# Kernel optimization log

Measured on AMD Instinct MI355X. Metric: run time of the kernel, lower is better.

Reference implementation:

```python
import jax, jax.numpy as jnp
import numpy as np

NODE_NUM = 2048
DIM_IN = 2
DIM_OUT = 64
CHEB_K = 2
EMBED_DIM = 16
BATCH = 16


def _sagc(x, E, w_pool, b_pool):
    """AGCRN-style adaptive graph conv. x: [B,N,C]; E: [N,e];
    w_pool: [e,K,C,O]; b_pool: [e,O]. Returns (out [B,N,O], A [N,N])."""
    n = E.shape[0]
    A = E @ E.T                                   # [N,N] raw (signed) similarity
    supports = jax.nn.softmax(jax.nn.relu(A), axis=1)
    s_list = [jnp.eye(n, dtype=x.dtype), supports]
    for _ in range(2, CHEB_K):
        s_list.append(2.0 * supports @ s_list[-1] - s_list[-2])
    S = jnp.stack(s_list[:CHEB_K])                # [K,N,N]
    W = jnp.einsum('ne,ekio->nkio', E, w_pool)    # per-node weights [N,K,C,O]
    b = E @ b_pool                                # [N,O]
    x_g = jnp.einsum('knm,bmi->bnki', S, x)       # [B,N,K,C]
    out = jnp.einsum('bnki,nkio->bno', x_g, W) + b
    return out, A


def _degrees(adj_mask, H, weight):
    """adj_mask: [N,N] {0,1}; H: [B,N,D]; weight: [N,N] -> softmaxed [B,N,N]."""
    HHT = jnp.einsum('bnd,bmd->bnm', H, H)        # [B,N,N]
    AHHT = adj_mask * HHT                          # broadcast [N,N]*[B,N,N]
    AHHTW = jnp.einsum('bnm,mk->bnk', AHHT, weight)
    return jax.nn.softmax(AHHTW, axis=-1)


def setup_inputs() -> dict:
    key = jax.random.key(0)
    ks = jax.random.split(key, 9)
    din = DIM_IN + DIM_OUT
    return {
        'x': jax.random.normal(ks[0], (BATCH, NODE_NUM, DIM_IN), jnp.float32),
        'state': jax.random.normal(ks[1], (BATCH, NODE_NUM, DIM_OUT), jnp.float32),
        'node_embeddings': jax.random.normal(ks[2], (NODE_NUM, EMBED_DIM), jnp.float32) * 0.5,
        'weight_connect': jax.random.normal(ks[3], (NODE_NUM, NODE_NUM), jnp.float32) * 0.02,
        'weight_disconnect': jax.random.normal(ks[4], (NODE_NUM, NODE_NUM), jnp.float32) * 0.02,
        'gate_w': jax.random.normal(ks[5], (EMBED_DIM, CHEB_K, din, 2 * DIM_OUT), jnp.float32) * 0.05,
        'gate_b': jax.random.normal(ks[6], (EMBED_DIM, 2 * DIM_OUT), jnp.float32) * 0.05,
        'upd_w': jax.random.normal(ks[7], (EMBED_DIM, CHEB_K, din, DIM_OUT), jnp.float32) * 0.05,
        'upd_b': jax.random.normal(ks[8], (EMBED_DIM, DIM_OUT), jnp.float32) * 0.05,
    }


def reference(x, state, node_embeddings, weight_connect, weight_disconnect,
              gate_w, gate_b, upd_w, upd_b):
    inp = jnp.concatenate([x, state], axis=-1)            # [B,N,Cin+D]
    x_gconv, A = _sagc(inp, node_embeddings, gate_w, gate_b)
    z_r = jax.nn.sigmoid(x_gconv)
    z, r = jnp.split(z_r, 2, axis=-1)
    candidate = jnp.concatenate([x, z * state], axis=-1)
    hc = jnp.tanh(_sagc(candidate, node_embeddings, upd_w, upd_b)[0])
    h = r * state + (1.0 - r) * hc                        # [B,N,D]
    A_connect = jnp.where(A > 0, 1.0, 0.0).astype(h.dtype)
    A_disconnect = jnp.where(A < 0, 1.0, 0.0).astype(h.dtype)
    deg_c = _degrees(A_connect, h, weight_connect)        # [B,N,N]
    deg_d = _degrees(A_disconnect, h, weight_disconnect)
    numerator = (0.8 * h
                 - 0.1 * jnp.einsum('bnm,bmd->bnd', deg_c, h)
                 + 0.1 * jnp.einsum('bnm,bmd->bnd', deg_d, h))
    return numerator
```

## Files before the change

### kernel.cpp

```cpp
#include <hip/hip_runtime.h>
#include <hip/hip_bf16.h>

typedef unsigned short u16;
typedef unsigned int   u32;
typedef unsigned char  u8;

typedef __attribute__((ext_vector_type(8))) short bf16x8;
typedef __attribute__((ext_vector_type(4))) float f32x4;
typedef __attribute__((ext_vector_type(16))) float f32x16;

static __device__ __forceinline__ float bf2f(u16 u){ return __uint_as_float(((u32)u)<<16); }
static __device__ __forceinline__ u16 f2bf(float f){
  u32 u = __float_as_uint(f);
  u32 r = (u + 0x7fff + ((u>>16)&1)) >> 16;
  return (u16)r;
}

static __device__ __forceinline__ u8 f2fp8(float v){
  v = fminf(440.f, fmaxf(-440.f, v));
  return (u8)(__builtin_amdgcn_cvt_pk_fp8_f32(v, 0.f, 0, false) & 0xff);
}
static __device__ __forceinline__ u32 pk4_fp8(float a, float b, float c, float d){
  int w = __builtin_amdgcn_cvt_pk_fp8_f32(a, b, 0, false);
  w = __builtin_amdgcn_cvt_pk_fp8_f32(c, d, w, true);
  return (u32)w;
}

static __device__ __forceinline__ f32x4 mfma_bf16(bf16x8 a, bf16x8 b, f32x4 c){
  return __builtin_amdgcn_mfma_f32_16x16x32_bf16(a, b, c, 0, 0, 0);
}
static __device__ __forceinline__ f32x16 mfma_bf16_32(bf16x8 a, bf16x8 b, f32x16 c){
  return __builtin_amdgcn_mfma_f32_32x32x16_bf16(a, b, c, 0, 0, 0);
}
static __device__ __forceinline__ f32x16 mfma_fp8_32(long a, long b, f32x16 c){
  return __builtin_amdgcn_mfma_f32_32x32x16_fp8_fp8(a, b, c, 0, 0, 0);
}
static __device__ __forceinline__ long lo64(uint4 v){ return (long)(((unsigned long long)v.y<<32) | v.x); }
static __device__ __forceinline__ long hi64(uint4 v){ return (long)(((unsigned long long)v.w<<32) | v.z); }
static __device__ __forceinline__ long mklong(u32 lo, u32 hi){ return (long)(((unsigned long long)hi<<32) | lo); }

__global__ void k_w8(const float* __restrict__ Wc, const float* __restrict__ Wd,
                     u8* __restrict__ Wc8, u8* __restrict__ Wd8){
  __shared__ float tile[64][65];
  const float* src = blockIdx.z ? Wd : Wc;
  u8* dst = blockIdx.z ? Wd8 : Wc8;
  const int m0 = blockIdx.x*64, k0 = blockIdx.y*64;
  const int t = threadIdx.x, r = t & 63, cc = t >> 6;
  #pragma unroll
  for (int j=0;j<4;j++){
    float4 v = *(const float4*)&src[(size_t)(m0+r)*2048 + k0 + cc*16 + j*4];
    tile[r][cc*16+j*4+0]=v.x; tile[r][cc*16+j*4+1]=v.y;
    tile[r][cc*16+j*4+2]=v.z; tile[r][cc*16+j*4+3]=v.w;
  }
  __syncthreads();
  const int lane = t & 63, sub = t >> 6;
  const int kth = sub & 1, mcp = sub >> 1;
  const int kl = kth*32 + (lane & 31);
  const int ml = mcp*32 + (lane >> 5)*8;
  u32 b0 = pk4_fp8(16.f*tile[ml+ 0][kl], 16.f*tile[ml+ 1][kl], 16.f*tile[ml+ 2][kl], 16.f*tile[ml+ 3][kl]);
  u32 b1 = pk4_fp8(16.f*tile[ml+ 4][kl], 16.f*tile[ml+ 5][kl], 16.f*tile[ml+ 6][kl], 16.f*tile[ml+ 7][kl]);
  u32 b2 = pk4_fp8(16.f*tile[ml+16][kl], 16.f*tile[ml+17][kl], 16.f*tile[ml+18][kl], 16.f*tile[ml+19][kl]);
  u32 b3 = pk4_fp8(16.f*tile[ml+20][kl], 16.f*tile[ml+21][kl], 16.f*tile[ml+22][kl], 16.f*tile[ml+23][kl]);
  const int pt = m0 >> 6, kt = (k0 >> 5) + kth;
  u8* dbase = dst + (size_t)((pt*64 + kt)*2 + mcp)*1024 + lane*16;
  *(uint4*)dbase = make_uint4(b0, b1, b2, b3);
}

__global__ void k_hcvt(const float* __restrict__ h, u16* __restrict__ hb16,
                       u8* __restrict__ ht8p, u16* __restrict__ hfm){
  __shared__ float tile[64][65];
  const int k0 = blockIdx.x*64, b = blockIdx.y;
  const int t = threadIdx.x, r = t & 63, cc = t >> 6;
  const float* src = h + ((size_t)b*2048 + k0)*64;
  u32 hw[8];
  #pragma unroll
  for (int j=0;j<4;j++){
    float4 v = *(const float4*)&src[(size_t)r*64 + cc*16 + j*4];
    tile[r][cc*16+j*4+0]=v.x; tile[r][cc*16+j*4+1]=v.y;
    tile[r][cc*16+j*4+2]=v.z; tile[r][cc*16+j*4+3]=v.w;
    hw[2*j]   = (u32)f2bf(v.x) | ((u32)f2bf(v.y)<<16);
    hw[2*j+1] = (u32)f2bf(v.z) | ((u32)f2bf(v.w)<<16);
  }
  u16* hp = hb16 + (((size_t)b*2048 + k0 + r)*64 + cc*16);
  *(uint4*)hp     = make_uint4(hw[0],hw[1],hw[2],hw[3]);
  *(uint4*)(hp+8) = make_uint4(hw[4],hw[5],hw[6],hw[7]);
  __syncthreads();
  {
    const int lane = t & 63, sub = cc;
    const int k16 = (k0 >> 4) + sub;
    const int lr = sub*16 + ((lane >> 5) << 3);
    const int d0 = lane & 31;
    #pragma unroll
    for (int dt=0; dt<2; ++dt){
      const int d = dt*32 + d0;
      u32 w0 = pk4_fp8(tile[lr+0][d], tile[lr+1][d], tile[lr+2][d], tile[lr+3][d]);
      u32 w1 = pk4_fp8(tile[lr+4][d], tile[lr+5][d], tile[lr+6][d], tile[lr+7][d]);
      *(uint2*)(ht8p + (size_t)b*131072 + (size_t)(k16*2 + dt)*512 + lane*8) = make_uint2(w0, w1);
    }
  }
  {
    const int col = k0 + r, ks = cc >> 1, q0 = (cc & 1)*2;
    const int ctg = col >> 4, lcv = col & 15;
    u16* fbase = hfm + (size_t)b*131072 + (size_t)ks*65536 + ((size_t)ctg*64)*8;
    #pragma unroll
    for (int qq=0; qq<2; ++qq){
      int q = q0 + qq;
      u32 p0 = (u32)f2bf(tile[r][ks*32+q*8+0]) | ((u32)f2bf(tile[r][ks*32+q*8+1])<<16);
      u32 p1 = (u32)f2bf(tile[r][ks*32+q*8+2]) | ((u32)f2bf(tile[r][ks*32+q*8+3])<<16);
      u32 p2 = (u32)f2bf(tile[r][ks*32+q*8+4]) | ((u32)f2bf(tile[r][ks*32+q*8+5])<<16);
      u32 p3 = (u32)f2bf(tile[r][ks*32+q*8+6]) | ((u32)f2bf(tile[r][ks*32+q*8+7])<<16);
      *(uint4*)(fbase + (size_t)(q*16 + lcv)*8) = make_uint4(p0,p1,p2,p3);
    }
  }
}

__global__ void k_P(const float* __restrict__ E, u16* __restrict__ P, u8* __restrict__ msk){
  __shared__ float Ew[16];
  __shared__ float arow[2048];
  __shared__ float red[4];
  const int t = threadIdx.x, n = blockIdx.x;
  if (t < 16) Ew[t] = E[n*16 + t];
  __syncthreads();
  float lmax = 0.f;
  for (int i=0;i<8;i++){
    int m = t + 256*i;
    const float* ep = E + m*16;
    float dot = 0.f;
    #pragma unroll
    for (int d=0; d<16; ++d) dot += Ew[d]*ep[d];
    msk[n*2048 + m] = dot > 0.f ? (u8)1 : (dot < 0.f ? (u8)2 : (u8)0);
    float ar = fmaxf(dot, 0.f);
    arow[m] = ar;
    lmax = fmaxf(lmax, ar);
  }
  for (int o=1;o<64;o<<=1) lmax = fmaxf(lmax, __shfl_xor(lmax, o));
  if ((t&63)==0) red[t>>6] = lmax;
  __syncthreads();
  float gmax = fmaxf(fmaxf(red[0],red[1]), fmaxf(red[2],red[3]));
  __syncthreads();
  float lsum = 0.f;
  for (int i=0;i<8;i++){
    int m = t + 256*i;
    float e = expf(arow[m] - gmax);
    arow[m] = e;
    lsum += e;
  }
  for (int o=1;o<64;o<<=1) lsum += __shfl_xor(lsum, o);
  if ((t&63)==0) red[t>>6] = lsum;
  __syncthreads();
  float inv = 1.f/(red[0]+red[1]+red[2]+red[3]);
  for (int i=0;i<8;i++){
    int m = t + 256*i;
    P[n*2048 + m] = f2bf(arow[m]*inv);
  }
}

__global__ void k_mbits(const u8* __restrict__ msk, u32* __restrict__ mp2, u32* __restrict__ mn2){
  const int m = blockIdx.x, nb = blockIdx.y*256;
  const int t = threadIdx.x, w = t>>6, lane = t&63;
  u8 v = msk[(size_t)(nb + t)*2048 + m];
  unsigned long long bp = __ballot(v == (u8)1);
  unsigned long long bn = __ballot(v == (u8)2);
  if (lane == 0){
    int wi = (nb + w*64) >> 5;
    mp2[(size_t)wi*2048 + m]     = (u32)bp;
    mp2[(size_t)(wi+1)*2048 + m] = (u32)(bp>>32);
    mn2[(size_t)wi*2048 + m]     = (u32)bn;
    mn2[(size_t)(wi+1)*2048 + m] = (u32)(bn>>32);
  }
}

__global__ void k_c1x(const u16* __restrict__ P, const float* __restrict__ x, float* __restrict__ c1x){
  const int t = threadIdx.x;
  const int r = t>>1, c = t&1;
  const int n = blockIdx.x*64 + r, b = blockIdx.y;
  const u16* pr = P + (size_t)n*2048;
  const float* xb = x + (size_t)b*2048*2 + c;
  float acc = 0.f;
  for (int m=0;m<2048;m+=4){
    acc += bf2f(pr[m+0])*xb[(m+0)*2];
    acc += bf2f(pr[m+1])*xb[(m+1)*2];
    acc += bf2f(pr[m+2])*xb[(m+2)*2];
    acc += bf2f(pr[m+3])*xb[(m+3)*2];
  }
  c1x[((size_t)b*2048 + n)*2 + c] = acc;
}

__global__ void k_conv(const u16* __restrict__ P, const float* __restrict__ Z, float* __restrict__ Y){
  __shared__ u16 Pt[64][68];
  __shared__ u16 Zhi[64][68];
  __shared__ u16 Zlo[64][68];
  const int t = threadIdx.x;
  const int w = t >> 6, lane = t & 63, l32 = lane & 31, h32 = lane >> 5;
  const int nh = w & 1, dh = w >> 1;
  const int n0 = blockIdx.x*64, b = blockIdx.y;
  const int mloc = t & 63, grp = t >> 6;
  f32x16 acch = (f32x16)(0.f), accl = (f32x16)(0.f);
  for (int mc = 0; mc < 32; ++mc){
    const int m0 = mc*64;
    {
      const u16* pp = P + (size_t)(n0 + mloc)*2048 + m0 + grp*16;
      uint4 v0 = *(const uint4*)pp;
      uint4 v1 = *(const uint4*)(pp + 8);
      *(uint4*)&Pt[mloc][grp*16]     = v0;
      *(uint4*)&Pt[mloc][grp*16 + 8] = v1;
      const float* zp = Z + ((size_t)b*2048 + m0 + mloc)*64 + grp*16;
      #pragma unroll
      for (int jj = 0; jj < 4; ++jj){
        float4 zv = *(const float4*)(zp + jj*4);
        const int dd = grp*16 + jj*4;
        u16 h0 = f2bf(zv.x); Zhi[dd+0][mloc] = h0; Zlo[dd+0][mloc] = f2bf(zv.x - bf2f(h0));
        u16 h1 = f2bf(zv.y); Zhi[dd+1][mloc] = h1; Zlo[dd+1][mloc] = f2bf(zv.y - bf2f(h1));
        u16 h2 = f2bf(zv.z); Zhi[dd+2][mloc] = h2; Zlo[dd+2][mloc] = f2bf(zv.z - bf2f(h2));
        u16 h3 = f2bf(zv.w); Zhi[dd+3][mloc] = h3; Zlo[dd+3][mloc] = f2bf(zv.w - bf2f(h3));
      }
    }
    __syncthreads();
    #pragma unroll
    for (int kt = 0; kt < 4; ++kt){
      bf16x8 a  = *(const bf16x8*)&Pt[nh*32 + l32][kt*16 + h32*8];
      bf16x8 bh = *(const bf16x8*)&Zhi[dh*32 + l32][kt*16 + h32*8];
      bf16x8 bl = *(const bf16x8*)&Zlo[dh*32 + l32][kt*16 + h32*8];
      acch = mfma_bf16_32(a, bh, acch);
      accl = mfma_bf16_32(a, bl, accl);
    }
    __syncthreads();
  }
  #pragma unroll
  for (int g = 0; g < 16; ++g){
    const int row = (g&3) + 8*(g>>2) + 4*h32;
    Y[((size_t)b*2048 + n0 + nh*32 + row)*64 + dh*32 + l32] = acch[g] + accl[g];
  }
}

__global__ void k_gate(const float* __restrict__ E, const float* __restrict__ gw, const float* __restrict__ gb,
                       const float* __restrict__ x, const float* __restrict__ state,
                       const float* __restrict__ c1x, const float* __restrict__ c1s,
                       float* __restrict__ zs, float* __restrict__ rws){
  __shared__ float Ew[16];
  __shared__ float bnv[128];
  __shared__ float Wn[2][66][64];
  __shared__ float xg4[4][2][66];
  const int t = threadIdx.x, n = blockIdx.x;
  if (t < 16) Ew[t] = E[n*16 + t];
  __syncthreads();
  if (t < 128){
    float a = 0.f;
    #pragma unroll
    for (int e=0;e<16;e++) a += Ew[e]*gb[e*128 + t];
    bnv[t] = a;
  }
  for (int half=0; half<2; ++half){
    for (int idx=t; idx<8448; idx+=256){
      int o = idx & 63, rest = idx>>6, i = rest % 66, k = rest / 66;
      float a = 0.f;
      #pragma unroll
      for (int e=0;e<16;e++) a += Ew[e]*gw[((e*2+k)*66 + i)*128 + half*64 + o];
      Wn[k][i][o] = a;
    }
    __syncthreads();
    for (int bb=0; bb<4; ++bb){
      for (int idx=t; idx<528; idx+=256){
        int bi = idx/132, rem = idx%132, k = rem/66, i = rem%66;
        int b = bb*4 + bi;
        float v;
        if (k==0) v = (i<2) ? x[((size_t)b*2048+n)*2 + i] : state[((size_t)b*2048+n)*64 + (i-2)];
        else      v = (i<2) ? c1x[((size_t)b*2048+n)*2 + i] : c1s[((size_t)b*2048+n)*64 + (i-2)];
        xg4[bi][k][i] = v;
      }
      __syncthreads();
      {
        int bi = t>>6, o = t&63, b = bb*4 + bi;
        float a = 0.f;
        #pragma unroll
        for (int k=0;k<2;k++)
          for (int i=0;i<66;i++) a += xg4[bi][k][i]*Wn[k][i][o];
        a += bnv[half*64 + o];
        float s = 1.f/(1.f + expf(-a));
        if (half==0) zs[((size_t)b*2048+n)*64 + o] = s*state[((size_t)b*2048+n)*64 + o];
        else         rws[((size_t)b*2048+n)*64 + o] = s;
      }
      __syncthreads();
    }
  }
}

__global__ void k_upd(const float* __restrict__ E, const float* __restrict__ uw, const float* __restrict__ ub,
                      const float* __restrict__ x, const float* __restrict__ state,
                      const float* __restrict__ zs, const float* __restrict__ c1x, const float* __restrict__ c2s,
                      const float* __restrict__ rws, float* __restrict__ h){
  __shared__ float Ew[16];
  __shared__ float bnu[64];
  __shared__ float Wn[2][66][64];
  __shared__ float xg4[4][2][66];
  const int t = threadIdx.x, n = blockIdx.x;
  if (t < 16) Ew[t] = E[n*16 + t];
  __syncthreads();
  if (t < 64){
    float a = 0.f;
    #pragma unroll
    for (int e=0;e<16;e++) a += Ew[e]*ub[e*64 + t];
    bnu[t] = a;
  }
  for (int idx=t; idx<8448; idx+=256){
    int o = idx & 63, rest = idx>>6, i = rest % 66, k = rest / 66;
    float a = 0.f;
    #pragma unroll
    for (int e=0;e<16;e++) a += Ew[e]*uw[((e*2+k)*66 + i)*64 + o];
    Wn[k][i][o] = a;
  }
  __syncthreads();
  for (int bb=0; bb<4; ++bb){
    for (int idx=t; idx<528; idx+=256){
      int bi = idx/132, rem = idx%132, k = rem/66, i = rem%66;
      int b = bb*4 + bi;
      float v;
      if (k==0) v = (i<2) ? x[((size_t)b*2048+n)*2 + i] : zs[((size_t)b*2048+n)*64 + (i-2)];
      else      v = (i<2) ? c1x[((size_t)b*2048+n)*2 + i] : c2s[((size_t)b*2048+n)*64 + (i-2)];
      xg4[bi][k][i] = v;
    }
    __syncthreads();
    {
      int bi = t>>6, o = t&63, b = bb*4 + bi;
      float a = 0.f;
      #pragma unroll
      for (int k=0;k<2;k++)
        for (int i=0;i<66;i++) a += xg4[bi][k][i]*Wn[k][i][o];
      float hc = tanhf(a + bnu[o]);
      float rv = rws[((size_t)b*2048+n)*64 + o];
      h[((size_t)b*2048+n)*64 + o] = rv*state[((size_t)b*2048+n)*64 + o] + (1.f - rv)*hc;
    }
    __syncthreads();
  }
}

static __device__ __forceinline__ void sm_step(f32x16& LK0, f32x16& LK1,
    f32x16& OA, f32x16& OB, float& mrun, float& srun,
    const u8* __restrict__ htb, int ktA, int ktB, int lane, int h32){
  const float LN256 = 5.545177444479562f;
  float cmax = LK0[0];
  #pragma unroll
  for (int g=1; g<16; ++g) cmax = fmaxf(cmax, LK0[g]);
  #pragma unroll
  for (int g=0; g<16; ++g) cmax = fmaxf(cmax, LK1[g]);
  cmax = fmaxf(cmax, __shfl_xor(cmax, 32));
  float mnew = fmaxf(mrun, 0.5f*cmax);
  float sc = __expf(mrun - mnew);
  srun *= sc;
  #pragma unroll
  for (int g=0; g<16; ++g){
    const int rowl = (g&3) + 8*(g>>2) + 4*h32;
    float fr = __shfl(sc, rowl);
    OA[g] *= fr; OB[g] *= fr;
  }
  float cs = 0.f;
  #pragma unroll
  for (int kti=0; kti<2; ++kti){
    const int kt = kti ? ktB : ktA;
    float p[16];
    #pragma unroll
    for (int g=0; g<16; ++g){
      float Lg = kti ? LK1[g] : LK0[g];
      p[g] = __expf(0.5f*Lg - mnew + LN256);
      cs += p[g];
    }
    u32 qA = pk4_fp8(p[0],p[1],p[2],p[3]);
    u32 qB = pk4_fp8(p[4],p[5],p[6],p[7]);
    u32 qC = pk4_fp8(p[8],p[9],p[10],p[11]);
    u32 qD = pk4_fp8(p[12],p[13],p[14],p[15]);
    u32 xA = __shfl_xor(qA,32), xB = __shfl_xor(qB,32);
    u32 xC = __shfl_xor(qC,32), xD = __shfl_xor(qD,32);
    long pf0 = h32 ? mklong(xB,qB) : mklong(qA,xA);
    long pf1 = h32 ? mklong(xD,qD) : mklong(qC,xC);
    long h00 = *(const long*)(htb + (size_t)((kt*2+0)*2 + 0)*512 + lane*8);
    long h01 = *(const long*)(htb + (size_t)((kt*2+0)*2 + 1)*512 + lane*8);
    long h10 = *(const long*)(htb + (size_t)((kt*2+1)*2 + 0)*512 + lane*8);
    long h11 = *(const long*)(htb + (size_t)((kt*2+1)*2 + 1)*512 + lane*8);
    OA = mfma_fp8_32(pf0, h00, OA);
    OB = mfma_fp8_32(pf0, h01, OB);
    OA = mfma_fp8_32(pf1, h10, OA);
    OB = mfma_fp8_32(pf1, h11, OB);
  }
  cs += __shfl_xor(cs, 32);
  srun += cs;
  mrun = mnew;
}

#define SROW8 2056

__global__ void __launch_bounds__(512,2) k_deg(
    const u32* __restrict__ mbits, const u16* __restrict__ hb16,
    const u8* __restrict__ W8,
    const u8* __restrict__ ht8p, const u16* __restrict__ hfm,
    const float* __restrict__ hf32, const float* __restrict__ oc_in,
    float* __restrict__ outp, int fin){
  extern __shared__ u8 S[];
  __shared__ float maxw[64][8];
  __shared__ float sumw[64][8];
  __shared__ float sgl_lds[64];
  const int t = threadIdx.x;
  const int w = t >> 6, lane = t & 63, lc = lane & 15, q = lane >> 4;
  const int l32 = lane & 31, h32 = lane >> 5;
  const int id = blockIdx.x;
  const int b = id >> 5, n0 = (id & 31) * 64;
  const int p0 = (id >> 3) & 31;
  const u32* mrow0 = mbits + (size_t)(n0 >> 5)*2048;
  const u32* mrow1 = mrow0 + 2048;
  const u16* hbb = hb16 + (size_t)b*2048*64;
  const u16* hfb = hfm + (size_t)b*131072;
  const u8* htb = ht8p + (size_t)b*131072;

  {
    const int c0 = p0 & 15;
    bf16x8 A[4][2];
    #pragma unroll
    for (int rt=0; rt<4; ++rt)
      #pragma unroll
      for (int ks=0; ks<2; ++ks)
        A[rt][ks] = *(const bf16x8*)&hbb[(size_t)(n0 + rt*16 + lc)*64 + ks*32 + q*8];
    int ctg0 = w*16 + c0;
    bf16x8 B0c = *(const bf16x8*)(hfb + (size_t)ctg0*512 + lane*8);
    bf16x8 B1c = *(const bf16x8*)(hfb + 65536 + (size_t)ctg0*512 + lane*8);
    u32 m0c = mrow0[ctg0*16 + lc], m1c = mrow1[ctg0*16 + lc];
    #pragma unroll 1
    for (int ct=0; ct<16; ++ct){
      const int ctg  = w*16 + ((ct + c0) & 15);
      const int ctgn = w*16 + ((ct + 1 + c0) & 15);
      bf16x8 B0n = *(const bf16x8*)(hfb + (size_t)ctgn*512 + lane*8);
      bf16x8 B1n = *(const bf16x8*)(hfb + 65536 + (size_t)ctgn*512 + lane*8);
      u32 m0n = mrow0[ctgn*16 + lc], m1n = mrow1[ctgn*16 + lc];
      const int mcol = ctg*16 + lc;
      f32x4 a[4];
      #pragma unroll
      for (int rt=0; rt<4; ++rt){
        a[rt] = (f32x4){0.f,0.f,0.f,0.f};
        a[rt] = mfma_bf16(A[rt][0], B0c, a[rt]);
        a[rt] = mfma_bf16(A[rt][1], B1c, a[rt]);
      }
      #pragma unroll
      for (int rt=0; rt<4; ++rt){
        const u32 mw = (rt < 2) ? m0c : m1c;
        #pragma unroll
        for (int i=0;i<4;i++){
          const int row = rt*16 + q*4 + i;
          float v = ((mw >> (row & 31)) & 1u) ? a[rt][i]*0.125f : 0.f;
          S[row*SROW8 + mcol] = f2fp8(v);
        }
      }
      B0c = B0n; B1c = B1n; m0c = m0n; m1c = m1n;
    }
  }
  __syncthreads();

  const u8* sb0 = S + (size_t)l32*SROW8 + h32*8;
  const u8* sb1 = S + (size_t)(32 + l32)*SROW8 + h32*8;
  const u8* wl = W8 + lane*16;
  f32x16 oA0 = (f32x16)(0.f), oA1 = (f32x16)(0.f);
  f32x16 oB0 = (f32x16)(0.f), oB1 = (f32x16)(0.f);
  float mrun0 = -1e30f, srun0 = 0.f, mrun1 = -1e30f, srun1 = 0.f;
  #pragma unroll 1
  for (int si = 0; si < 4; ++si){
    const int ktA = w*8 + si*2, ktB = ktA + 1;
    f32x16 L00 = (f32x16)(0.f), L01 = (f32x16)(0.f);
    f32x16 L10 = (f32x16)(0.f), L11 = (f32x16)(0.f);
    uint4 wv0, wv1, wv2, wv3;
    {
      const int pt0 = p0;
      wv0 = *(const uint4*)(wl + (size_t)((pt0*64 + ktA)*2 + 0)*1024);
      wv1 = *(const uint4*)(wl + (size_t)((pt0*64 + ktA)*2 + 1)*1024);
      wv2 = *(const uint4*)(wl + (size_t)((pt0*64 + ktB)*2 + 0)*1024);
      wv3 = *(const uint4*)(wl + (size_t)((pt0*64 + ktB)*2 + 1)*1024);
    }
    __builtin_amdgcn_s_setprio(1);
    #pragma unroll 1
    for (int pti = 0; pti < 32; ++pti){
      const int pt  = (pti + p0) & 31;
      const int ptn = (pti + 1 + p0) & 31;
      long b00 = *(const long*)(sb0 + pt*64 +  0);
      long b01 = *(const long*)(sb0 + pt*64 + 16);
      long b02 = *(const long*)(sb0 + pt*64 + 32);
      long b03 = *(const long*)(sb0 + pt*64 + 48);
      long b10 = *(const long*)(sb1 + pt*64 +  0);
      long b11 = *(const long*)(sb1 + pt*64 + 16);
      long b12 = *(const long*)(sb1 + pt*64 + 32);
      long b13 = *(const long*)(sb1 + pt*64 + 48);
      uint4 wn0 = *(const uint4*)(wl + (size_t)((ptn*64 + ktA)*2 + 0)*1024);
      uint4 wn1 = *(const uint4*)(wl + (size_t)((ptn*64 + ktA)*2 + 1)*1024);
      uint4 wn2 = *(const uint4*)(wl + (size_t)((ptn*64 + ktB)*2 + 0)*1024);
      uint4 wn3 = *(const uint4*)(wl + (size_t)((ptn*64 + ktB)*2 + 1)*1024);
      L00 = mfma_fp8_32(lo64(wv0), b00, L00);
      L01 = mfma_fp8_32(lo64(wv0), b10, L01);
      L10 = mfma_fp8_32(lo64(wv2), b00, L10);
      L11 = mfma_fp8_32(lo64(wv2), b10, L11);
      L00 = mfma_fp8_32(hi64(wv0), b01, L00);
      L01 = mfma_fp8_32(hi64(wv0), b11, L01);
      L10 = mfma_fp8_32(hi64(wv2), b01, L10);
      L11 = mfma_fp8_32(hi64(wv2), b11, L11);
      L00 = mfma_fp8_32(lo64(wv1), b02, L00);
      L01 = mfma_fp8_32(lo64(wv1), b12, L01);
      L10 = mfma_fp8_32(lo64(wv3), b02, L10);
      L11 = mfma_fp8_32(lo64(wv3), b12, L11);
      L00 = mfma_fp8_32(hi64(wv1), b03, L00);
      L01 = mfma_fp8_32(hi64(wv1), b13, L01);
      L10 = mfma_fp8_32(hi64(wv3), b03, L10);
      L11 = mfma_fp8_32(hi64(wv3), b13, L11);
      wv0 = wn0; wv1 = wn1; wv2 = wn2; wv3 = wn3;
    }
    __builtin_amdgcn_s_setprio(0);
    sm_step(L00, L10, oA0, oA1, mrun0, srun0, htb, ktA, ktB, lane, h32);
    sm_step(L01, L11, oB0, oB1, mrun1, srun1, htb, ktA, ktB, lane, h32);
  }

  if (h32 == 0){
    maxw[l32][w] = mrun0;      sumw[l32][w] = srun0;
    maxw[32 + l32][w] = mrun1; sumw[32 + l32][w] = srun1;
  }
  __syncthreads();
  float* scr = (float*)S;
  {
    float m_g0 = maxw[l32][0];
    #pragma unroll
    for (int j=1;j<8;j++) m_g0 = fmaxf(m_g0, maxw[l32][j]);
    float s_g0 = 0.f;
    #pragma unroll
    for (int j=0;j<8;j++) s_g0 += sumw[l32][j]*__expf(maxw[l32][j]-m_g0);
    float m_g1 = maxw[32+l32][0];
    #pragma unroll
    for (int j=1;j<8;j++) m_g1 = fmaxf(m_g1, maxw[32+l32][j]);
    float s_g1 = 0.f;
    #pragma unroll
    for (int j=0;j<8;j++) s_g1 += sumw[32+l32][j]*__expf(maxw[32+l32][j]-m_g1);
    if (w == 0 && h32 == 0){
      sgl_lds[l32] = s_g0;
      sgl_lds[32 + l32] = s_g1;
    }
    float f0 = __expf(mrun0 - m_g0);
    float f1 = __expf(mrun1 - m_g1);
    #pragma unroll
    for (int g=0; g<16; ++g){
      const int rowl = (g&3) + 8*(g>>2) + 4*h32;
      float fr0 = __shfl(f0, rowl);
      float fr1 = __shfl(f1, rowl);
      scr[((size_t)w*64 + rowl)*64 + l32]           = oA0[g]*fr0;
      scr[((size_t)w*64 + rowl)*64 + 32 + l32]      = oA1[g]*fr0;
      scr[((size_t)w*64 + 32 + rowl)*64 + l32]      = oB0[g]*fr1;
      scr[((size_t)w*64 + 32 + rowl)*64 + 32 + l32] = oB1[g]*fr1;
    }
  }
  __syncthreads();

  {
    const int n_g = t >> 3, d0 = (t & 7)*8;
    const float sdiv = sgl_lds[n_g];
    float* op = outp + (size_t)b*2048*64;
    const float* hp = hf32 + (size_t)b*2048*64;
    const float* cp = oc_in + (size_t)b*2048*64;
    #pragma unroll
    for (int j=0;j<8;j++){
      const int d = d0 + j;
      float v = 0.f;
      #pragma unroll
      for (int qq=0; qq<8; ++qq)
        v += scr[((size_t)qq*64 + n_g)*64 + d];
      v /= sdiv;
      size_t idx = (size_t)(n0 + n_g)*64 + d;
      if (fin) v = 0.8f*hp[idx] - 0.1f*cp[idx] + 0.1f*v;
      op[idx] = v;
    }
  }
}

extern "C" void kernel_launch(void* const* d_in, const int* in_sizes, int n_in,
                              void* d_out, int out_size, void* d_ws, size_t ws_size,
                              hipStream_t stream) {
  const float* x     = (const float*)d_in[0];
  const float* state = (const float*)d_in[1];
  const float* E     = (const float*)d_in[2];
  const float* Wc    = (const float*)d_in[3];
  const float* Wd    = (const float*)d_in[4];
  const float* gw    = (const float*)d_in[5];
  const float* gb    = (const float*)d_in[6];
  const float* uw    = (const float*)d_in[7];
  const float* ub    = (const float*)d_in[8];

  char* base = (char*)d_ws;
  u16*   P    = (u16*)(base + 0);
  u32*   mp2  = (u32*)(base + 0);
  u32*   mn2  = (u32*)(base + 524288);
  u8*    msk  = (u8*) (base + 8388608);
  u8*    Wc8  = (u8*) (base + 12582912);
  u8*    Wd8  = (u8*) (base + 16777216);
  u16*   hb16 = (u16*)(base + 20971520);
  u8*    ht8p = (u8*) (base + 25165824);
  u16*   hfm  = (u16*)(base + 27262976);
  float* c1x  = (float*)(base + 31457280);
  float* c1s  = (float*)(base + 31719424);
  float* zs   = (float*)(base + 40108032);
  float* rws  = (float*)(base + 48496640);
  float* c2s  = (float*)(base + 56885248);
  float* h    = (float*)(base + 65273856);
  float* oc   = c1s;
  float* od   = c2s;

  k_w8<<<dim3(32,32,2), 256, 0, stream>>>(Wc, Wd, Wc8, Wd8);
  k_P<<<2048, 256, 0, stream>>>(E, P, msk);
  k_c1x<<<dim3(32,16), 128, 0, stream>>>(P, x, c1x);
  k_conv<<<dim3(32,16), 256, 0, stream>>>(P, state, c1s);
  k_gate<<<2048, 256, 0, stream>>>(E, gw, gb, x, state, c1x, c1s, zs, rws);
  k_conv<<<dim3(32,16), 256, 0, stream>>>(P, zs, c2s);
  k_upd<<<2048, 256, 0, stream>>>(E, uw, ub, x, state, zs, c1x, c2s, rws, h);
  k_hcvt<<<dim3(32,16), 256, 0, stream>>>(h, hb16, ht8p, hfm);
  k_mbits<<<dim3(2048,8), 256, 0, stream>>>(msk, mp2, mn2);

  const int deg_lds = 64*SROW8;
  hipFuncSetAttribute((const void*)k_deg, hipFuncAttributeMaxDynamicSharedMemorySize, deg_lds);
  k_deg<<<512, 512, deg_lds, stream>>>(mp2, hb16, Wc8, ht8p, hfm, h, h, oc, 0);
  k_deg<<<512, 512, deg_lds, stream>>>(mn2, hb16, Wd8, ht8p, hfm, h, oc, (float*)d_out, 1);
}
```

Baseline: 1.029 ms.

## Fuse c1x into conv, tile mask bit-packing, interleave softmax steps, vectorize P dot

Folds the P·x product into the first conv kernel so P is read once, dropping a separate kernel launch. Rewrites mask bit-packing to stage a 256x64 byte tile in LDS, replacing a strided byte gather with one block per column. Merges the two online-softmax steps in the degree kernel into one function so the two independent chains interleave for more ILP, at the cost of register pressure. Vectorizes the embedding dot in k_P with float4 loads.

```diff
diff --git a/kernel.cpp b/kernel.cpp
--- a/kernel.cpp
+++ b/kernel.cpp
@@ -124,10 +124,12 @@
   float lmax = 0.f;
   for (int i=0;i<8;i++){
     int m = t + 256*i;
-    const float* ep = E + m*16;
-    float dot = 0.f;
-    #pragma unroll
-    for (int d=0; d<16; ++d) dot += Ew[d]*ep[d];
+    const float4* ep = (const float4*)(E + m*16);
+    float4 e0 = ep[0], e1 = ep[1], e2 = ep[2], e3 = ep[3];
+    float dot = e0.x*Ew[0] + e0.y*Ew[1] + e0.z*Ew[2] + e0.w*Ew[3]
+              + e1.x*Ew[4] + e1.y*Ew[5] + e1.z*Ew[6] + e1.w*Ew[7]
+              + e2.x*Ew[8] + e2.y*Ew[9] + e2.z*Ew[10] + e2.w*Ew[11]
+              + e3.x*Ew[12] + e3.y*Ew[13] + e3.z*Ew[14] + e3.w*Ew[15];
     msk[n*2048 + m] = dot > 0.f ? (u8)1 : (dot < 0.f ? (u8)2 : (u8)0);
     float ar = fmaxf(dot, 0.f);
     arow[m] = ar;
@@ -156,46 +158,47 @@
 }
 
 __global__ void k_mbits(const u8* __restrict__ msk, u32* __restrict__ mp2, u32* __restrict__ mn2){
-  const int m = blockIdx.x, nb = blockIdx.y*256;
-  const int t = threadIdx.x, w = t>>6, lane = t&63;
-  u8 v = msk[(size_t)(nb + t)*2048 + m];
-  unsigned long long bp = __ballot(v == (u8)1);
-  unsigned long long bn = __ballot(v == (u8)2);
-  if (lane == 0){
-    int wi = (nb + w*64) >> 5;
-    mp2[(size_t)wi*2048 + m]     = (u32)bp;
-    mp2[(size_t)(wi+1)*2048 + m] = (u32)(bp>>32);
-    mn2[(size_t)wi*2048 + m]     = (u32)bn;
-    mn2[(size_t)(wi+1)*2048 + m] = (u32)(bn>>32);
-  }
-}
-
-__global__ void k_c1x(const u16* __restrict__ P, const float* __restrict__ x, float* __restrict__ c1x){
+  __shared__ u8 tile[256][72];
+  const int m0 = blockIdx.x*64, n0 = blockIdx.y*256;
   const int t = threadIdx.x;
-  const int r = t>>1, c = t&1;
-  const int n = blockIdx.x*64 + r, b = blockIdx.y;
-  const u16* pr = P + (size_t)n*2048;
-  const float* xb = x + (size_t)b*2048*2 + c;
-  float acc = 0.f;
-  for (int m=0;m<2048;m+=4){
-    acc += bf2f(pr[m+0])*xb[(m+0)*2];
-    acc += bf2f(pr[m+1])*xb[(m+1)*2];
-    acc += bf2f(pr[m+2])*xb[(m+2)*2];
-    acc += bf2f(pr[m+3])*xb[(m+3)*2];
-  }
-  c1x[((size_t)b*2048 + n)*2 + c] = acc;
-}
-
-__global__ void k_conv(const u16* __restrict__ P, const float* __restrict__ Z, float* __restrict__ Y){
+  {
+    const u8* src = msk + (size_t)(n0 + t)*2048 + m0;
+    #pragma unroll
+    for (int j=0;j<8;j++)
+      *(uint2*)&tile[t][j*8] = *(const uint2*)(src + j*8);
+  }
+  __syncthreads();
+  const int m = t & 63, g = t >> 6;
+  #pragma unroll
+  for (int jj=0; jj<2; ++jj){
+    const int j = g + jj*4;
+    u32 bp = 0, bn = 0;
+    #pragma unroll
+    for (int i=0;i<32;++i){
+      u8 v = tile[j*32 + i][m];
+      bp |= (u32)(v == (u8)1) << i;
+      bn |= (u32)(v == (u8)2) << i;
+    }
+    const size_t wi = (size_t)((n0 >> 5) + j)*2048 + m0 + m;
+    mp2[wi] = bp;
+    mn2[wi] = bn;
+  }
+}
+
+__global__ void k_conv(const u16* __restrict__ P, const float* __restrict__ Z, float* __restrict__ Y,
+                       const float* __restrict__ x, float* __restrict__ c1x, int withx){
   __shared__ u16 Pt[64][68];
   __shared__ u16 Zhi[64][68];
   __shared__ u16 Zlo[64][68];
+  __shared__ float xt[64][2];
   const int t = threadIdx.x;
   const int w = t >> 6, lane = t & 63, l32 = lane & 31, h32 = lane >> 5;
   const int nh = w & 1, dh = w >> 1;
   const int n0 = blockIdx.x*64, b = blockIdx.y;
   const int mloc = t & 63, grp = t >> 6;
   f32x16 acch = (f32x16)(0.f), accl = (f32x16)(0.f);
+  float xacc = 0.f;
+  const int xnl = t >> 2, xc = (t >> 1) & 1, xmh = t & 1;
   for (int mc = 0; mc < 32; ++mc){
     const int m0 = mc*64;
     {
@@ -214,6 +217,8 @@
         u16 h2 = f2bf(zv.z); Zhi[dd+2][mloc] = h2; Zlo[dd+2][mloc] = f2bf(zv.z - bf2f(h2));
         u16 h3 = f2bf(zv.w); Zhi[dd+3][mloc] = h3; Zlo[dd+3][mloc] = f2bf(zv.w - bf2f(h3));
       }
+      if (withx && t < 128)
+        xt[t>>1][t&1] = x[((size_t)b*2048 + m0 + (t>>1))*2 + (t&1)];
     }
     __syncthreads();
     #pragma unroll
@@ -224,12 +229,24 @@
       acch = mfma_bf16_32(a, bh, acch);
       accl = mfma_bf16_32(a, bl, accl);
     }
+    if (withx){
+      #pragma unroll
+      for (int mi = 0; mi < 32; ++mi){
+        const int ml = xmh*32 + mi;
+        xacc += bf2f(Pt[xnl][ml])*xt[ml][xc];
+      }
+    }
     __syncthreads();
   }
   #pragma unroll
   for (int g = 0; g < 16; ++g){
     const int row = (g&3) + 8*(g>>2) + 4*h32;
     Y[((size_t)b*2048 + n0 + nh*32 + row)*64 + dh*32 + l32] = acch[g] + accl[g];
+  }
+  if (withx){
+    float o = xacc + __shfl_xor(xacc, 1);
+    if (xmh == 0)
+      c1x[((size_t)b*2048 + n0 + xnl)*2 + xc] = o;
   }
 }
 
@@ -334,56 +351,78 @@
   }
 }
 
-static __device__ __forceinline__ void sm_step(f32x16& LK0, f32x16& LK1,
-    f32x16& OA, f32x16& OB, float& mrun, float& srun,
+static __device__ __forceinline__ void sm_step2(
+    f32x16& L00, f32x16& L10, f32x16& L01, f32x16& L11,
+    f32x16& oA0, f32x16& oA1, f32x16& oB0, f32x16& oB1,
+    float& mrun0, float& srun0, float& mrun1, float& srun1,
     const u8* __restrict__ htb, int ktA, int ktB, int lane, int h32){
   const float LN256 = 5.545177444479562f;
-  float cmax = LK0[0];
-  #pragma unroll
-  for (int g=1; g<16; ++g) cmax = fmaxf(cmax, LK0[g]);
-  #pragma unroll
-  for (int g=0; g<16; ++g) cmax = fmaxf(cmax, LK1[g]);
-  cmax = fmaxf(cmax, __shfl_xor(cmax, 32));
-  float mnew = fmaxf(mrun, 0.5f*cmax);
-  float sc = __expf(mrun - mnew);
-  srun *= sc;
+  float c0 = L00[0], c1 = L01[0];
+  #pragma unroll
+  for (int g=1; g<16; ++g){ c0 = fmaxf(c0, L00[g]); c1 = fmaxf(c1, L01[g]); }
+  #pragma unroll
+  for (int g=0; g<16; ++g){ c0 = fmaxf(c0, L10[g]); c1 = fmaxf(c1, L11[g]); }
+  c0 = fmaxf(c0, __shfl_xor(c0, 32));
+  c1 = fmaxf(c1, __shfl_xor(c1, 32));
+  float mnew0 = fmaxf(mrun0, 0.5f*c0);
+  float mnew1 = fmaxf(mrun1, 0.5f*c1);
+  float sc0 = __expf(mrun0 - mnew0);
+  float sc1 = __expf(mrun1 - mnew1);
+  srun0 *= sc0; srun1 *= sc1;
   #pragma unroll
   for (int g=0; g<16; ++g){
     const int rowl = (g&3) + 8*(g>>2) + 4*h32;
-    float fr = __shfl(sc, rowl);
-    OA[g] *= fr; OB[g] *= fr;
-  }
-  float cs = 0.f;
+    float f0 = __shfl(sc0, rowl);
+    float f1 = __shfl(sc1, rowl);
+    oA0[g] *= f0; oA1[g] *= f0;
+    oB0[g] *= f1; oB1[g] *= f1;
+  }
+  float cs0 = 0.f, cs1 = 0.f;
   #pragma unroll
   for (int kti=0; kti<2; ++kti){
     const int kt = kti ? ktB : ktA;
-    float p[16];
-    #pragma unroll
-    for (int g=0; g<16; ++g){
-      float Lg = kti ? LK1[g] : LK0[g];
-      p[g] = __expf(0.5f*Lg - mnew + LN256);
-      cs += p[g];
-    }
-    u32 qA = pk4_fp8(p[0],p[1],p[2],p[3]);
-    u32 qB = pk4_fp8(p[4],p[5],p[6],p[7]);
-    u32 qC = pk4_fp8(p[8],p[9],p[10],p[11]);
-    u32 qD = pk4_fp8(p[12],p[13],p[14],p[15]);
-    u32 xA = __shfl_xor(qA,32), xB = __shfl_xor(qB,32);
-    u32 xC = __shfl_xor(qC,32), xD = __shfl_xor(qD,32);
-    long pf0 = h32 ? mklong(xB,qB) : mklong(qA,xA);
-    long pf1 = h32 ? mklong(xD,qD) : mklong(qC,xC);
     long h00 = *(const long*)(htb + (size_t)((kt*2+0)*2 + 0)*512 + lane*8);
     long h01 = *(const long*)(htb + (size_t)((kt*2+0)*2 + 1)*512 + lane*8);
     long h10 = *(const long*)(htb + (size_t)((kt*2+1)*2 + 0)*512 + lane*8);
     long h11 = *(const long*)(htb + (size_t)((kt*2+1)*2 + 1)*512 + lane*8);
-    OA = mfma_fp8_32(pf0, h00, OA);
-    OB = mfma_fp8_32(pf0, h01, OB);
-    OA = mfma_fp8_32(pf1, h10, OA);
-    OB = mfma_fp8_32(pf1, h11, OB);
-  }
-  cs += __shfl_xor(cs, 32);
-  srun += cs;
-  mrun = mnew;
+    float p0[16], p1[16];
+    #pragma unroll
+    for (int g=0; g<16; ++g){
+      float La = kti ? L10[g] : L00[g];
+      float Lb = kti ? L11[g] : L01[g];
+      p0[g] = __expf(0.5f*La - mnew0 + LN256);
+      p1[g] = __expf(0.5f*Lb - mnew1 + LN256);
+      cs0 += p0[g]; cs1 += p1[g];
+    }
+    u32 qA0 = pk4_fp8(p0[0],p0[1],p0[2],p0[3]);
+    u32 qB0 = pk4_fp8(p0[4],p0[5],p0[6],p0[7]);
+    u32 qC0 = pk4_fp8(p0[8],p0[9],p0[10],p0[11]);
+    u32 qD0 = pk4_fp8(p0[12],p0[13],p0[14],p0[15]);
+    u32 qA1 = pk4_fp8(p1[0],p1[1],p1[2],p1[3]);
+    u32 qB1 = pk4_fp8(p1[4],p1[5],p1[6],p1[7]);
+    u32 qC1 = pk4_fp8(p1[8],p1[9],p1[10],p1[11]);
+    u32 qD1 = pk4_fp8(p1[12],p1[13],p1[14],p1[15]);
+    u32 xA0 = __shfl_xor(qA0,32), xB0 = __shfl_xor(qB0,32);
+    u32 xC0 = __shfl_xor(qC0,32), xD0 = __shfl_xor(qD0,32);
+    u32 xA1 = __shfl_xor(qA1,32), xB1 = __shfl_xor(qB1,32);
+    u32 xC1 = __shfl_xor(qC1,32), xD1 = __shfl_xor(qD1,32);
+    long pf00 = h32 ? mklong(xB0,qB0) : mklong(qA0,xA0);
+    long pf01 = h32 ? mklong(xD0,qD0) : mklong(qC0,xC0);
+    long pf10 = h32 ? mklong(xB1,qB1) : mklong(qA1,xA1);
+    long pf11 = h32 ? mklong(xD1,qD1) : mklong(qC1,xC1);
+    oA0 = mfma_fp8_32(pf00, h00, oA0);
+    oA1 = mfma_fp8_32(pf00, h01, oA1);
+    oB0 = mfma_fp8_32(pf10, h00, oB0);
+    oB1 = mfma_fp8_32(pf10, h01, oB1);
+    oA0 = mfma_fp8_32(pf01, h10, oA0);
+    oA1 = mfma_fp8_32(pf01, h11, oA1);
+    oB0 = mfma_fp8_32(pf11, h10, oB0);
+    oB1 = mfma_fp8_32(pf11, h11, oB1);
+  }
+  cs0 += __shfl_xor(cs0, 32);
+  cs1 += __shfl_xor(cs1, 32);
+  srun0 += cs0; srun1 += cs1;
+  mrun0 = mnew0; mrun1 = mnew1;
 }
 
 #define SROW8 2056
@@ -507,8 +546,8 @@
       wv0 = wn0; wv1 = wn1; wv2 = wn2; wv3 = wn3;
     }
     __builtin_amdgcn_s_setprio(0);
-    sm_step(L00, L10, oA0, oA1, mrun0, srun0, htb, ktA, ktB, lane, h32);
-    sm_step(L01, L11, oB0, oB1, mrun1, srun1, htb, ktA, ktB, lane, h32);
+    sm_step2(L00, L10, L01, L11, oA0, oA1, oB0, oB1,
+             mrun0, srun0, mrun1, srun1, htb, ktA, ktB, lane, h32);
   }
 
   if (h32 == 0){
@@ -600,17 +639,15 @@
   float* c2s  = (float*)(base + 56885248);
   float* h    = (float*)(base + 65273856);
   float* oc   = c1s;
-  float* od   = c2s;
 
   k_w8<<<dim3(32,32,2), 256, 0, stream>>>(Wc, Wd, Wc8, Wd8);
   k_P<<<2048, 256, 0, stream>>>(E, P, msk);
-  k_c1x<<<dim3(32,16), 128, 0, stream>>>(P, x, c1x);
-  k_conv<<<dim3(32,16), 256, 0, stream>>>(P, state, c1s);
+  k_conv<<<dim3(32,16), 256, 0, stream>>>(P, state, c1s, x, c1x, 1);
   k_gate<<<2048, 256, 0, stream>>>(E, gw, gb, x, state, c1x, c1s, zs, rws);
-  k_conv<<<dim3(32,16), 256, 0, stream>>>(P, zs, c2s);
+  k_conv<<<dim3(32,16), 256, 0, stream>>>(P, zs, c2s, x, c1x, 0);
   k_upd<<<2048, 256, 0, stream>>>(E, uw, ub, x, state, zs, c1x, c2s, rws, h);
   k_hcvt<<<dim3(32,16), 256, 0, stream>>>(h, hb16, ht8p, hfm);
-  k_mbits<<<dim3(2048,8), 256, 0, stream>>>(msk, mp2, mn2);
+  k_mbits<<<dim3(32,8), 256, 0, stream>>>(msk, mp2, mn2);
 
   const int deg_lds = 64*SROW8;
   hipFuncSetAttribute((const void*)k_deg, hipFuncAttributeMaxDynamicSharedMemorySize, deg_lds);
```

After: 996.4 us, median of 2. 1.03x faster.
